# Performance work log

Measured on AMD Instinct MI355X. Metric: run time of the kernel, lower is better.

## Reference

```python
import jax, jax.numpy as jnp
import numpy as np

EMBED_DIM = 1024
NUM_HEADS = 16
HEAD_DIM = EMBED_DIM // NUM_HEADS  # 64
TOKEN_GRID = 48
TASK_ROPE_TOKENS = 8
SEQ_LEN = TASK_ROPE_TOKENS + TOKEN_GRID * TOKEN_GRID  # 2312
ROT_DIM = HEAD_DIM // 2  # 32, rotary 'dim' arg
SCALE = HEAD_DIM ** -0.5


def _make_rope_tables():
    # Faithful to RotaryEmbedding.__init__
    freqs = 1.0 / 10000.0 ** (jnp.arange(0, ROT_DIM, 2, dtype=jnp.float32) / float(ROT_DIM))
    t = jnp.arange(TOKEN_GRID, dtype=jnp.float32) / float(TOKEN_GRID) * float(TOKEN_GRID)
    freqs_1d = jnp.einsum('i,f->if', t, freqs)          # [G, ROT_DIM/2]
    freqs_1d = jnp.repeat(freqs_1d, 2, axis=-1)          # [G, ROT_DIM]
    fh = jnp.broadcast_to(freqs_1d[:, None, :], (TOKEN_GRID, TOKEN_GRID, ROT_DIM))
    fw = jnp.broadcast_to(freqs_1d[None, :, :], (TOKEN_GRID, TOKEN_GRID, ROT_DIM))
    freqs_2d = jnp.concatenate([fh, fw], axis=-1)        # [G, G, HEAD_DIM]
    freqs_flat = freqs_2d.reshape(TOKEN_GRID * TOKEN_GRID, -1)
    return jnp.cos(freqs_flat), jnp.sin(freqs_flat)      # each [G*G, HEAD_DIM]


def _rotate_half(x):
    x1, x2 = jnp.split(x, 2, axis=-1)
    return jnp.concatenate([-x2, x1], axis=-1)


def _apply_rope(t, cos, sin):
    # t: [H, L, D]; rotate tokens after the task prefix
    usable = t.shape[1] - TASK_ROPE_TOKENS
    c = cos[:usable, :HEAD_DIM]
    s = sin[:usable, :HEAD_DIM]
    to_rotate = t[:, TASK_ROPE_TOKENS:, :HEAD_DIM]
    rotated = to_rotate * c + _rotate_half(to_rotate) * s
    prefix = t[:, :TASK_ROPE_TOKENS, :HEAD_DIM]
    return jnp.concatenate([prefix, rotated], axis=1)


def setup_inputs() -> dict:
    key = jax.random.key(0)
    k1, k2, k3, k4, k5 = jax.random.split(key, 5)
    cos, sin = _make_rope_tables()
    bound = 1.0 / np.sqrt(EMBED_DIM)
    return {
        'x': jax.random.normal(k1, (SEQ_LEN, EMBED_DIM), dtype=jnp.float32),
        'key_padding_mask': jnp.ones((SEQ_LEN,), dtype=bool),
        'qkv_w': jax.random.uniform(k2, (3 * EMBED_DIM, EMBED_DIM), minval=-bound, maxval=bound, dtype=jnp.float32),
        'qkv_b': jax.random.uniform(k3, (3 * EMBED_DIM,), minval=-bound, maxval=bound, dtype=jnp.float32),
        'proj_w': jax.random.uniform(k4, (EMBED_DIM, EMBED_DIM), minval=-bound, maxval=bound, dtype=jnp.float32),
        'proj_b': jax.random.uniform(k5, (EMBED_DIM,), minval=-bound, maxval=bound, dtype=jnp.float32),
        'freqs_cos': cos,
        'freqs_sin': sin,
    }


def reference(x, key_padding_mask, qkv_w, qkv_b, proj_w, proj_b, freqs_cos, freqs_sin):
    L = x.shape[0]
    qkv = x @ qkv_w.T + qkv_b                             # [L, 3E]
    qkv = qkv.reshape(L, 3, NUM_HEADS, HEAD_DIM)
    qkv = jnp.transpose(qkv, (1, 2, 0, 3))                # [3, H, L, D]
    q, k, v = qkv[0], qkv[1], qkv[2]
    q = _apply_rope(q, freqs_cos, freqs_sin)
    k = _apply_rope(k, freqs_cos, freqs_sin)
    scores = jnp.einsum('hld,hmd->hlm', q, k) * SCALE     # [H, L, L]
    scores = jnp.where(key_padding_mask[None, None, :], scores, jnp.finfo(scores.dtype).min)
    weights = jax.nn.softmax(scores, axis=-1)
    context = jnp.einsum('hij,hjd->hid', weights, v)      # [H, L, D]
    context = jnp.transpose(context, (1, 0, 2)).reshape(L, -1)  # [L, E]
    out = context @ proj_w.T + proj_b
    return out
```

## Files before the change

### kernel.cpp

```cpp
#include <hip/hip_runtime.h>
#include <hip/hip_bf16.h>

#define SEQ   2312
#define EMB   1024
#define NH    16
#define HD    64
#define LP    2368
#define NKT   37
#define KSPLIT0 19
#define QKVN  3072
#define QSCALE 0.1803368801111713f

typedef __bf16 bf16x8 __attribute__((ext_vector_type(8)));
typedef __bf16 bf16x4 __attribute__((ext_vector_type(4)));
typedef _Float16 f16x8 __attribute__((ext_vector_type(8)));
typedef _Float16 f16x4 __attribute__((ext_vector_type(4)));
typedef float  f32x4  __attribute__((ext_vector_type(4)));

#define MFMA16(a,b,c) __builtin_amdgcn_mfma_f32_16x16x32_bf16((a),(b),(c),0,0,0)

#define N1 (SEQ * EMB / 4)
#define N2 (QKVN * EMB / 4)
#define N3 (EMB * EMB / 4)

__global__ __launch_bounds__(256) void cast_all_kernel(const float* __restrict__ x,
                                                       const float* __restrict__ qkv_w,
                                                       const float* __restrict__ proj_w,
                                                       __bf16* __restrict__ xb,
                                                       __bf16* __restrict__ wqkvb,
                                                       __bf16* __restrict__ wprojb) {
  int i = blockIdx.x * 256 + threadIdx.x;
  const float* src; __bf16* dst; int j;
  if (i < N1)           { src = x;      dst = xb;     j = i; }
  else if (i < N1 + N2) { src = qkv_w;  dst = wqkvb;  j = i - N1; }
  else if (i < N1 + N2 + N3) { src = proj_w; dst = wprojb; j = i - N1 - N2; }
  else return;
  const float4 v = reinterpret_cast<const float4*>(src)[j];
  bf16x4 o = { (__bf16)v.x, (__bf16)v.y, (__bf16)v.z, (__bf16)v.w };
  reinterpret_cast<bf16x4*>(dst)[j] = o;
}

__device__ __forceinline__ bf16x8 lds_frag(const __bf16* __restrict__ buf, int row, int cb) {
  const char* p = (const char*)buf + row * 128 + (cb ^ ((row & 7) << 4));
  return *reinterpret_cast<const bf16x8*>(p);
}

__device__ __forceinline__ void gl_lds16(const char* g, char* l) {
  __builtin_amdgcn_global_load_lds(
      (const __attribute__((address_space(1))) void*)g,
      (__attribute__((address_space(3))) void*)l, 16, 0, 0);
}

template <bool OUT_BF16>
__global__ __launch_bounds__(256) void gemm_lds_kernel(const __bf16* __restrict__ A,
                                                       const __bf16* __restrict__ B,
                                                       const float* __restrict__ bias,
                                                       void* __restrict__ Cout,
                                                       int M, int N, int K, int MT) {
  const int g = ((int)blockIdx.x & 7) * ((int)gridDim.x >> 3) + ((int)blockIdx.x >> 3);
  const int mt = g % MT, nt = g / MT;
  const int t = threadIdx.x;
  const int wid = t >> 6;
  const int lane = t & 63;
  const int lr = lane & 15, lg = lane >> 4;
  const int mrow = (wid >> 1) * 64, ncol = (wid & 1) * 64;

  __shared__ __bf16 sbuf[2][2][128 * 64];

  const int srow = t >> 3;
  const int ksw  = ((t & 7) ^ (srow & 7)) * 8;
  const __bf16* asrc[4]; const __bf16* bsrc[4];
#pragma unroll
  for (int i = 0; i < 4; ++i) {
    const int row = i * 32 + srow;
    int arow = mt * 128 + row; if (arow >= M) arow = M - 1;
    asrc[i] = A + (size_t)arow * K + ksw;
    bsrc[i] = B + (size_t)(nt * 128 + row) * K + ksw;
  }

  auto issue = [&](int buf, int kk) {
    char* ab = (char*)sbuf[buf][0] + wid * 1024;
    char* bb = (char*)sbuf[buf][1] + wid * 1024;
#pragma unroll
    for (int i = 0; i < 4; ++i) gl_lds16((const char*)(asrc[i] + kk), ab + i * 4096);
#pragma unroll
    for (int i = 0; i < 4; ++i) gl_lds16((const char*)(bsrc[i] + kk), bb + i * 4096);
  };

  f32x4 acc[4][4] = {};
  const int NK = K >> 6;
  issue(0, 0);

  for (int ks = 0; ks < NK; ++ks) {
    asm volatile("s_waitcnt vmcnt(0)" ::: "memory");
    __syncthreads();
    if (ks + 1 < NK) issue((ks + 1) & 1, (ks + 1) << 6);
    const __bf16* ab = sbuf[ks & 1][0];
    const __bf16* bb = sbuf[ks & 1][1];
#pragma unroll
    for (int kh2 = 0; kh2 < 2; ++kh2) {
      bf16x8 af[4], bf[4];
#pragma unroll
      for (int m = 0; m < 4; ++m) af[m] = lds_frag(ab, mrow + m * 16 + lr, kh2 * 64 + lg * 16);
#pragma unroll
      for (int n = 0; n < 4; ++n) bf[n] = lds_frag(bb, ncol + n * 16 + lr, kh2 * 64 + lg * 16);
#pragma unroll
      for (int m = 0; m < 4; ++m)
#pragma unroll
        for (int n = 0; n < 4; ++n)
          acc[m][n] = MFMA16(af[m], bf[n], acc[m][n]);
    }
    __syncthreads();
  }

#pragma unroll
  for (int m = 0; m < 4; ++m) {
#pragma unroll
    for (int n = 0; n < 4; ++n) {
#pragma unroll
      for (int r = 0; r < 4; ++r) {
        int row = mt * 128 + mrow + m * 16 + lg * 4 + r;
        int col = nt * 128 + ncol + n * 16 + lr;
        if (row < M) {
          float v = acc[m][n][r] + bias[col];
          if (OUT_BF16) reinterpret_cast<__bf16*>(Cout)[(size_t)row * N + col] = (__bf16)v;
          else          reinterpret_cast<float*>(Cout)[(size_t)row * N + col] = v;
        }
      }
    }
  }
}

__global__ __launch_bounds__(512) void gemm_qkv_kernel(const __bf16* __restrict__ A,
                                                       const __bf16* __restrict__ B,
                                                       const float* __restrict__ bias,
                                                       const float* __restrict__ fcos,
                                                       const float* __restrict__ fsin,
                                                       __bf16* __restrict__ qh,
                                                       __bf16* __restrict__ kh,
                                                       __bf16* __restrict__ vt) {
  const int g = ((int)blockIdx.x & 7) * 30 + ((int)blockIdx.x >> 3);
  const int mt = g % 10, nt = g / 10;
  const int t = threadIdx.x;
  const int wid = t >> 6;
  const int lane = t & 63;
  const int lr = lane & 15, lg = lane >> 4;
  const int mrow = (wid >> 1) * 64;
  const int ncol = (wid & 1) * 64;

  __shared__ __bf16 smem[49152];

  const int srow = t >> 3;
  const int ksw  = ((t & 7) ^ (srow & 7)) * 8;
  const __bf16* asrc[4]; const __bf16* bsrc[2];
#pragma unroll
  for (int i = 0; i < 4; ++i) {
    int arow = mt * 256 + i * 64 + srow; if (arow >= SEQ) arow = SEQ - 1;
    asrc[i] = A + (size_t)arow * EMB + ksw;
  }
#pragma unroll
  for (int i = 0; i < 2; ++i)
    bsrc[i] = B + (size_t)(nt * 128 + i * 64 + srow) * EMB + ksw;

  auto issue = [&](int buf, int kk) {
    char* ab = (char*)(smem + buf * 16384) + wid * 1024;
    char* bb = (char*)(smem + 32768 + buf * 8192) + wid * 1024;
#pragma unroll
    for (int i = 0; i < 4; ++i) gl_lds16((const char*)(asrc[i] + kk), ab + i * 8192);
#pragma unroll
    for (int i = 0; i < 2; ++i) gl_lds16((const char*)(bsrc[i] + kk), bb + i * 8192);
  };

  f32x4 acc[4][4] = {};
  issue(0, 0);

  for (int ks = 0; ks < 16; ++ks) {
    asm volatile("s_waitcnt vmcnt(0)" ::: "memory");
    __syncthreads();
    if (ks + 1 < 16) issue((ks + 1) & 1, (ks + 1) << 6);
    const __bf16* ab = smem + (ks & 1) * 16384;
    const __bf16* bb = smem + 32768 + (ks & 1) * 8192;
#pragma unroll
    for (int kh2 = 0; kh2 < 2; ++kh2) {
      bf16x8 af[4], bf[4];
#pragma unroll
      for (int m = 0; m < 4; ++m) af[m] = lds_frag(ab, mrow + m * 16 + lr, kh2 * 64 + lg * 16);
#pragma unroll
      for (int n = 0; n < 4; ++n) bf[n] = lds_frag(bb, ncol + n * 16 + lr, kh2 * 64 + lg * 16);
#pragma unroll
      for (int m = 0; m < 4; ++m)
#pragma unroll
        for (int n = 0; n < 4; ++n)
          acc[m][n] = MFMA16(af[m], bf[n], acc[m][n]);
    }
    __syncthreads();
  }

  const int colbase = nt * 128 + ncol;
  const int hb   = colbase >> 6;
  const int kind = hb >> 4;
  const int h    = hb & 15;
  float bb4[4];
#pragma unroll
  for (int n = 0; n < 4; ++n) bb4[n] = bias[colbase + n * 16 + lr];

  if (kind < 2) {
    __bf16* dst = (kind == 0 ? qh : kh) + (size_t)h * LP * 64;
    const float sc = (kind == 0) ? QSCALE : 1.0f;
#pragma unroll
    for (int m = 0; m < 4; ++m) {
#pragma unroll
      for (int r = 0; r < 4; ++r) {
        const int row = mt * 256 + mrow + m * 16 + lg * 4 + r;
        if (row >= SEQ) continue;
        float v0 = acc[m][0][r] + bb4[0];
        float v1 = acc[m][1][r] + bb4[1];
        float v2 = acc[m][2][r] + bb4[2];
        float v3 = acc[m][3][r] + bb4[3];
        if (row >= 8) {
          const float* cr = fcos + (size_t)(row - 8) * 64;
          const float* sr = fsin + (size_t)(row - 8) * 64;
          const float c0 = cr[lr],      s0 = sr[lr];
          const float c1 = cr[16 + lr], s1 = sr[16 + lr];
          const float c2 = cr[32 + lr], s2 = sr[32 + lr];
          const float c3 = cr[48 + lr], s3 = sr[48 + lr];
          const float o0 = v0 * c0 - v2 * s0;
          const float o2 = v2 * c2 + v0 * s2;
          const float o1 = v1 * c1 - v3 * s1;
          const float o3 = v3 * c3 + v1 * s3;
          v0 = o0; v1 = o1; v2 = o2; v3 = o3;
        }
        __bf16* p = dst + (size_t)row * 64;
        p[lr]      = (__bf16)(v0 * sc);
        p[16 + lr] = (__bf16)(v1 * sc);
        p[32 + lr] = (__bf16)(v2 * sc);
        p[48 + lr] = (__bf16)(v3 * sc);
      }
    }
  } else {
    __syncthreads();
    __bf16 (*vtile)[66] = reinterpret_cast<__bf16(*)[66]>(smem + wid * 64 * 66);
#pragma unroll
    for (int m = 0; m < 4; ++m)
#pragma unroll
      for (int r = 0; r < 4; ++r) {
        const int rl = m * 16 + lg * 4 + r;
#pragma unroll
        for (int n = 0; n < 4; ++n)
          vtile[rl][n * 16 + lr] = (__bf16)(acc[m][n][r] + bb4[n]);
      }
    __builtin_amdgcn_wave_barrier();
    const int pos = mt * 256 + mrow + lane;
    __bf16* vdst = vt + (size_t)h * 64 * LP;
    if (pos < LP) {
#pragma unroll 4
      for (int dl = 0; dl < 64; ++dl)
        vdst[(size_t)dl * LP + pos] = vtile[lane][dl];
    }
  }
}

__global__ __launch_bounds__(256) void flash_kernel(const __bf16* __restrict__ qh,
                                                    const __bf16* __restrict__ kh,
                                                    const __bf16* __restrict__ vt,
                                                    _Float16* __restrict__ Op,
                                                    float* __restrict__ lp) {
  const int g = (blockIdx.x & 7) * 148 + (blockIdx.x >> 3);
  const int h = g / 74;
  const int rem = g - h * 74;
  const int qb = rem >> 1, sp = rem & 1;
  const int kt0 = sp ? KSPLIT0 : 0, ktend = sp ? NKT : KSPLIT0;
  const int t = threadIdx.x;
  const int wid = t >> 6;
  const int lane = t & 63;
  const int lr = lane & 15, lg = lane >> 4;
  const int q0 = qb * 64 + wid * 16;

  __shared__ __bf16 kbuf[64 * 64];
  __shared__ __bf16 vbuf[64 * 64];
  __shared__ __bf16 plds[4][16][72];

  const __bf16* qbase = qh + ((size_t)h * LP + q0) * HD;
  const bf16x8 aq0 = *reinterpret_cast<const bf16x8*>(qbase + lr * HD + lg * 8);
  const bf16x8 aq1 = *reinterpret_cast<const bf16x8*>(qbase + lr * HD + 32 + lg * 8);

  const __bf16* khead = kh + (size_t)h * LP * HD;
  const __bf16* vhead = vt + (size_t)h * HD * LP;

  const int krow0 = t >> 3,        kcb0 = (t & 7) * 16;
  const int krow1 = 32 + (t >> 3);
  const int vrow  = t >> 2,        vcb0 = (t & 3) * 32;
  const int koff0 = krow0 * 128 + (kcb0 ^ ((krow0 & 7) << 4));
  const int koff1 = krow1 * 128 + (kcb0 ^ ((krow1 & 7) << 4));
  const int voff0 = vrow * 128 + (vcb0 ^ ((vrow & 7) << 4));
  const int voff1 = vrow * 128 + ((vcb0 + 16) ^ ((vrow & 7) << 4));
  const __bf16* vsrc = vhead + (size_t)vrow * LP + (t & 3) * 16;

  bf16x8 kreg0, kreg1, vreg0, vreg1;
  auto stage_load = [&](int kt) {
    const __bf16* kb = khead + (size_t)kt * 64 * HD;
    kreg0 = *reinterpret_cast<const bf16x8*>(kb + t * 8);
    kreg1 = *reinterpret_cast<const bf16x8*>(kb + 2048 + t * 8);
    vreg0 = *reinterpret_cast<const bf16x8*>(vsrc + kt * 64);
    vreg1 = *reinterpret_cast<const bf16x8*>(vsrc + kt * 64 + 8);
  };

  float l = 0.f;
  f32x4 oacc[4] = {};

  stage_load(kt0);

  for (int kt = kt0; kt < ktend; ++kt) {
    __syncthreads();
    *reinterpret_cast<bf16x8*>((char*)kbuf + koff0) = kreg0;
    *reinterpret_cast<bf16x8*>((char*)kbuf + koff1) = kreg1;
    *reinterpret_cast<bf16x8*>((char*)vbuf + voff0) = vreg0;
    *reinterpret_cast<bf16x8*>((char*)vbuf + voff1) = vreg1;
    __syncthreads();
    if (kt + 1 < ktend) stage_load(kt + 1);

    f32x4 sacc[4] = {};
    __builtin_amdgcn_s_setprio(1);
#pragma unroll
    for (int cg = 0; cg < 4; ++cg) {
      sacc[cg] = MFMA16(lds_frag(kbuf, cg * 16 + lr, lg * 16),      aq0, sacc[cg]);
      sacc[cg] = MFMA16(lds_frag(kbuf, cg * 16 + lr, 64 + lg * 16), aq1, sacc[cg]);
    }
    __builtin_amdgcn_s_setprio(0);
    if (kt == NKT - 1) {
#pragma unroll
      for (int cg = 0; cg < 4; ++cg)
#pragma unroll
        for (int r = 0; r < 4; ++r)
          if (kt * 64 + cg * 16 + lg * 4 + r >= SEQ) sacc[cg][r] = -1e30f;
    }
#pragma unroll
    for (int cg = 0; cg < 4; ++cg)
#pragma unroll
      for (int r = 0; r < 4; ++r) sacc[cg][r] = exp2f(sacc[cg][r]);
    float s0 = (sacc[0][0] + sacc[0][1]) + (sacc[0][2] + sacc[0][3]);
    float s1 = (sacc[1][0] + sacc[1][1]) + (sacc[1][2] + sacc[1][3]);
    float s2 = (sacc[2][0] + sacc[2][1]) + (sacc[2][2] + sacc[2][3]);
    float s3 = (sacc[3][0] + sacc[3][1]) + (sacc[3][2] + sacc[3][3]);
    l += (s0 + s1) + (s2 + s3);
#pragma unroll
    for (int cg = 0; cg < 4; ++cg) {
      bf16x4 pk = { (__bf16)sacc[cg][0], (__bf16)sacc[cg][1],
                    (__bf16)sacc[cg][2], (__bf16)sacc[cg][3] };
      *reinterpret_cast<bf16x4*>(&plds[wid][lr][cg * 16 + lg * 4]) = pk;
    }
    __builtin_amdgcn_wave_barrier();
    const bf16x8 ap0 = *reinterpret_cast<const bf16x8*>(&plds[wid][lr][lg * 8]);
    const bf16x8 ap1 = *reinterpret_cast<const bf16x8*>(&plds[wid][lr][32 + lg * 8]);
    __builtin_amdgcn_s_setprio(1);
#pragma unroll
    for (int cg = 0; cg < 4; ++cg) {
      oacc[cg] = MFMA16(lds_frag(vbuf, cg * 16 + lr, lg * 16),      ap0, oacc[cg]);
      oacc[cg] = MFMA16(lds_frag(vbuf, cg * 16 + lr, 64 + lg * 16), ap1, oacc[cg]);
    }
    __builtin_amdgcn_s_setprio(0);
  }
  float ltot = l;
  ltot += __shfl_xor(ltot, 16, 64);
  ltot += __shfl_xor(ltot, 32, 64);
  const float inv = 1.0f / ltot;
  const size_t rbase = ((size_t)sp * NH + h) * LP;
  if (lg == 0) lp[rbase + q0 + lr] = ltot;
  _Float16* orow = Op + (rbase + q0 + lr) * 64 + lg * 4;
#pragma unroll
  for (int cg = 0; cg < 4; ++cg) {
    f16x4 ov = { (_Float16)(oacc[cg][0] * inv), (_Float16)(oacc[cg][1] * inv),
                 (_Float16)(oacc[cg][2] * inv), (_Float16)(oacc[cg][3] * inv) };
    *reinterpret_cast<f16x4*>(orow + cg * 16) = ov;
  }
}

__global__ __launch_bounds__(256) void merge_kernel(const _Float16* __restrict__ Op,
                                                    const float* __restrict__ lp,
                                                    __bf16* __restrict__ ctx) {
  const int tg = blockIdx.x * 256 + threadIdx.x;
  const int rid = tg >> 2;
  const int d0 = (tg & 3) << 4;
  const int h = rid / LP;
  const int row = rid - h * LP;
  if (row >= SEQ) return;
  const size_t i0 = (size_t)h * LP + row;
  const size_t i1 = (size_t)NH * LP + i0;
  float w0 = lp[i0], w1 = lp[i1];
  const float inv = 1.0f / (w0 + w1);
  w0 *= inv; w1 *= inv;
  const f16x8* o0 = reinterpret_cast<const f16x8*>(Op + i0 * 64 + d0);
  const f16x8* o1 = reinterpret_cast<const f16x8*>(Op + i1 * 64 + d0);
  __bf16* co = ctx + (size_t)row * EMB + h * 64 + d0;
#pragma unroll
  for (int v = 0; v < 2; ++v) {
    const f16x8 a = o0[v], b = o1[v];
    bf16x8 o;
#pragma unroll
    for (int j = 0; j < 8; ++j)
      o[j] = (__bf16)((float)a[j] * w0 + (float)b[j] * w1);
    reinterpret_cast<bf16x8*>(co)[v] = o;
  }
}

extern "C" void kernel_launch(void* const* d_in, const int* in_sizes, int n_in,
                              void* d_out, int out_size, void* d_ws, size_t ws_size,
                              hipStream_t stream) {
  const float* x      = (const float*)d_in[0];
  const float* qkv_w  = (const float*)d_in[2];
  const float* qkv_b  = (const float*)d_in[3];
  const float* proj_w = (const float*)d_in[4];
  const float* proj_b = (const float*)d_in[5];
  const float* fcos   = (const float*)d_in[6];
  const float* fsin   = (const float*)d_in[7];
  float* out = (float*)d_out;

  char* ws = (char*)d_ws;
  size_t off = 0;
  auto alloc = [&](size_t bytes) {
    char* p = ws + off;
    off += (bytes + 255) & ~size_t(255);
    return p;
  };
  __bf16* xb     = (__bf16*)alloc((size_t)SEQ * EMB * 2);
  __bf16* wqkvb  = (__bf16*)alloc((size_t)QKVN * EMB * 2);
  __bf16* wprojb = (__bf16*)alloc((size_t)EMB * EMB * 2);
  __bf16* qh     = (__bf16*)alloc((size_t)NH * LP * HD * 2);
  __bf16* kh     = (__bf16*)alloc((size_t)NH * LP * HD * 2);
  __bf16* vtr    = (__bf16*)alloc((size_t)NH * HD * LP * 2);
  __bf16* ctx    = (__bf16*)alloc((size_t)SEQ * EMB * 2);
  _Float16* Op   = (_Float16*)alloc((size_t)2 * NH * LP * 64 * 2);
  float*    lpv  = (float*)alloc((size_t)2 * NH * LP * 4);

  cast_all_kernel<<<(N1 + N2 + N3 + 255) / 256, 256, 0, stream>>>(
      x, qkv_w, proj_w, xb, wqkvb, wprojb);

  gemm_qkv_kernel<<<240, 512, 0, stream>>>(xb, wqkvb, qkv_b, fcos, fsin, qh, kh, vtr);
  flash_kernel<<<1184, 256, 0, stream>>>(qh, kh, vtr, Op, lpv);
  merge_kernel<<<592, 256, 0, stream>>>(Op, lpv, ctx);
  gemm_lds_kernel<false><<<152, 256, 0, stream>>>(ctx, wprojb, proj_b, out,
                                                  SEQ, EMB, EMB, 19);
}
```

Before: 114.7 us.

## Fuse split-KV merge into output projection GEMM and compute row sums via MFMA

The separate merge kernel is removed, and the projection GEMM now loads both split-K partial outputs plus their softmax denominators, combines them in registers, and writes the merged bf16 A tile into LDS. This drops one launch and the ctx round trip through global memory. The A operand now goes through registers instead of direct global-to-LDS loads, which may add latency and register pressure. Separately, the flash kernel gets each softmax row sum from an extra pair of MFMAs against a ones vector, replacing the VALU adds and cross-lane shuffles.

```diff
diff --git a/kernel.cpp b/kernel.cpp
--- a/kernel.cpp
+++ b/kernel.cpp
@@ -49,86 +49,6 @@
   __builtin_amdgcn_global_load_lds(
       (const __attribute__((address_space(1))) void*)g,
       (__attribute__((address_space(3))) void*)l, 16, 0, 0);
-}
-
-template <bool OUT_BF16>
-__global__ __launch_bounds__(256) void gemm_lds_kernel(const __bf16* __restrict__ A,
-                                                       const __bf16* __restrict__ B,
-                                                       const float* __restrict__ bias,
-                                                       void* __restrict__ Cout,
-                                                       int M, int N, int K, int MT) {
-  const int g = ((int)blockIdx.x & 7) * ((int)gridDim.x >> 3) + ((int)blockIdx.x >> 3);
-  const int mt = g % MT, nt = g / MT;
-  const int t = threadIdx.x;
-  const int wid = t >> 6;
-  const int lane = t & 63;
-  const int lr = lane & 15, lg = lane >> 4;
-  const int mrow = (wid >> 1) * 64, ncol = (wid & 1) * 64;
-
-  __shared__ __bf16 sbuf[2][2][128 * 64];
-
-  const int srow = t >> 3;
-  const int ksw  = ((t & 7) ^ (srow & 7)) * 8;
-  const __bf16* asrc[4]; const __bf16* bsrc[4];
-#pragma unroll
-  for (int i = 0; i < 4; ++i) {
-    const int row = i * 32 + srow;
-    int arow = mt * 128 + row; if (arow >= M) arow = M - 1;
-    asrc[i] = A + (size_t)arow * K + ksw;
-    bsrc[i] = B + (size_t)(nt * 128 + row) * K + ksw;
-  }
-
-  auto issue = [&](int buf, int kk) {
-    char* ab = (char*)sbuf[buf][0] + wid * 1024;
-    char* bb = (char*)sbuf[buf][1] + wid * 1024;
-#pragma unroll
-    for (int i = 0; i < 4; ++i) gl_lds16((const char*)(asrc[i] + kk), ab + i * 4096);
-#pragma unroll
-    for (int i = 0; i < 4; ++i) gl_lds16((const char*)(bsrc[i] + kk), bb + i * 4096);
-  };
-
-  f32x4 acc[4][4] = {};
-  const int NK = K >> 6;
-  issue(0, 0);
-
-  for (int ks = 0; ks < NK; ++ks) {
-    asm volatile("s_waitcnt vmcnt(0)" ::: "memory");
-    __syncthreads();
-    if (ks + 1 < NK) issue((ks + 1) & 1, (ks + 1) << 6);
-    const __bf16* ab = sbuf[ks & 1][0];
-    const __bf16* bb = sbuf[ks & 1][1];
-#pragma unroll
-    for (int kh2 = 0; kh2 < 2; ++kh2) {
-      bf16x8 af[4], bf[4];
-#pragma unroll
-      for (int m = 0; m < 4; ++m) af[m] = lds_frag(ab, mrow + m * 16 + lr, kh2 * 64 + lg * 16);
-#pragma unroll
-      for (int n = 0; n < 4; ++n) bf[n] = lds_frag(bb, ncol + n * 16 + lr, kh2 * 64 + lg * 16);
-#pragma unroll
-      for (int m = 0; m < 4; ++m)
-#pragma unroll
-        for (int n = 0; n < 4; ++n)
-          acc[m][n] = MFMA16(af[m], bf[n], acc[m][n]);
-    }
-    __syncthreads();
-  }
-
-#pragma unroll
-  for (int m = 0; m < 4; ++m) {
-#pragma unroll
-    for (int n = 0; n < 4; ++n) {
-#pragma unroll
-      for (int r = 0; r < 4; ++r) {
-        int row = mt * 128 + mrow + m * 16 + lg * 4 + r;
-        int col = nt * 128 + ncol + n * 16 + lr;
-        if (row < M) {
-          float v = acc[m][n][r] + bias[col];
-          if (OUT_BF16) reinterpret_cast<__bf16*>(Cout)[(size_t)row * N + col] = (__bf16)v;
-          else          reinterpret_cast<float*>(Cout)[(size_t)row * N + col] = v;
-        }
-      }
-    }
-  }
 }
 
 __global__ __launch_bounds__(512) void gemm_qkv_kernel(const __bf16* __restrict__ A,
@@ -284,6 +204,9 @@
   const bf16x8 aq0 = *reinterpret_cast<const bf16x8*>(qbase + lr * HD + lg * 8);
   const bf16x8 aq1 = *reinterpret_cast<const bf16x8*>(qbase + lr * HD + 32 + lg * 8);
 
+  const bf16x8 vone = { (__bf16)1.f, (__bf16)1.f, (__bf16)1.f, (__bf16)1.f,
+                        (__bf16)1.f, (__bf16)1.f, (__bf16)1.f, (__bf16)1.f };
+
   const __bf16* khead = kh + (size_t)h * LP * HD;
   const __bf16* vhead = vt + (size_t)h * HD * LP;
 
@@ -305,7 +228,7 @@
     vreg1 = *reinterpret_cast<const bf16x8*>(vsrc + kt * 64 + 8);
   };
 
-  float l = 0.f;
+  f32x4 lacc = {};
   f32x4 oacc[4] = {};
 
   stage_load(kt0);
@@ -338,11 +261,6 @@
     for (int cg = 0; cg < 4; ++cg)
 #pragma unroll
       for (int r = 0; r < 4; ++r) sacc[cg][r] = exp2f(sacc[cg][r]);
-    float s0 = (sacc[0][0] + sacc[0][1]) + (sacc[0][2] + sacc[0][3]);
-    float s1 = (sacc[1][0] + sacc[1][1]) + (sacc[1][2] + sacc[1][3]);
-    float s2 = (sacc[2][0] + sacc[2][1]) + (sacc[2][2] + sacc[2][3]);
-    float s3 = (sacc[3][0] + sacc[3][1]) + (sacc[3][2] + sacc[3][3]);
-    l += (s0 + s1) + (s2 + s3);
 #pragma unroll
     for (int cg = 0; cg < 4; ++cg) {
       bf16x4 pk = { (__bf16)sacc[cg][0], (__bf16)sacc[cg][1],
@@ -358,11 +276,11 @@
       oacc[cg] = MFMA16(lds_frag(vbuf, cg * 16 + lr, lg * 16),      ap0, oacc[cg]);
       oacc[cg] = MFMA16(lds_frag(vbuf, cg * 16 + lr, 64 + lg * 16), ap1, oacc[cg]);
     }
+    lacc = MFMA16(vone, ap0, lacc);
+    lacc = MFMA16(vone, ap1, lacc);
     __builtin_amdgcn_s_setprio(0);
   }
-  float ltot = l;
-  ltot += __shfl_xor(ltot, 16, 64);
-  ltot += __shfl_xor(ltot, 32, 64);
+  const float ltot = lacc[0];
   const float inv = 1.0f / ltot;
   const size_t rbase = ((size_t)sp * NH + h) * LP;
   if (lg == 0) lp[rbase + q0 + lr] = ltot;
@@ -375,31 +293,105 @@
   }
 }
 
-__global__ __launch_bounds__(256) void merge_kernel(const _Float16* __restrict__ Op,
-                                                    const float* __restrict__ lp,
-                                                    __bf16* __restrict__ ctx) {
-  const int tg = blockIdx.x * 256 + threadIdx.x;
-  const int rid = tg >> 2;
-  const int d0 = (tg & 3) << 4;
-  const int h = rid / LP;
-  const int row = rid - h * LP;
-  if (row >= SEQ) return;
-  const size_t i0 = (size_t)h * LP + row;
-  const size_t i1 = (size_t)NH * LP + i0;
-  float w0 = lp[i0], w1 = lp[i1];
-  const float inv = 1.0f / (w0 + w1);
-  w0 *= inv; w1 *= inv;
-  const f16x8* o0 = reinterpret_cast<const f16x8*>(Op + i0 * 64 + d0);
-  const f16x8* o1 = reinterpret_cast<const f16x8*>(Op + i1 * 64 + d0);
-  __bf16* co = ctx + (size_t)row * EMB + h * 64 + d0;
-#pragma unroll
-  for (int v = 0; v < 2; ++v) {
-    const f16x8 a = o0[v], b = o1[v];
-    bf16x8 o;
-#pragma unroll
-    for (int j = 0; j < 8; ++j)
-      o[j] = (__bf16)((float)a[j] * w0 + (float)b[j] * w1);
-    reinterpret_cast<bf16x8*>(co)[v] = o;
+__global__ __launch_bounds__(256) void proj_merge_kernel(const _Float16* __restrict__ Op,
+                                                         const float* __restrict__ lp,
+                                                         const __bf16* __restrict__ B,
+                                                         const float* __restrict__ bias,
+                                                         float* __restrict__ Cout) {
+  const int g = ((int)blockIdx.x & 7) * 19 + ((int)blockIdx.x >> 3);
+  const int mt = g % 19, nt = g / 19;
+  const int t = threadIdx.x;
+  const int wid = t >> 6;
+  const int lane = t & 63;
+  const int lr = lane & 15, lg = lane >> 4;
+  const int mrow = (wid >> 1) * 64, ncol = (wid & 1) * 64;
+
+  __shared__ __bf16 sbuf[2][2][128 * 64];
+
+  const int srow = t >> 3;
+  const int ksw  = ((t & 7) ^ (srow & 7)) * 8;
+  int arows[4]; int adst[4]; const __bf16* bsrc[4];
+#pragma unroll
+  for (int i = 0; i < 4; ++i) {
+    const int row = i * 32 + srow;
+    int ar = mt * 128 + row; if (ar >= SEQ) ar = SEQ - 1;
+    arows[i] = ar;
+    adst[i] = row * 128 + (t & 7) * 16;
+    bsrc[i] = B + (size_t)(nt * 128 + row) * EMB + ksw;
+  }
+
+  auto issueB = [&](int buf, int kk) {
+    char* bb = (char*)sbuf[buf][1] + wid * 1024;
+#pragma unroll
+    for (int i = 0; i < 4; ++i) gl_lds16((const char*)(bsrc[i] + kk), bb + i * 4096);
+  };
+
+  f16x8 a0[4], a1[4]; float w0[4], w1[4];
+  auto loadA = [&](int ks) {
+#pragma unroll
+    for (int i = 0; i < 4; ++i) {
+      const size_t i0 = (size_t)ks * LP + arows[i];
+      const size_t i1 = (size_t)(NH + ks) * LP + arows[i];
+      a0[i] = *reinterpret_cast<const f16x8*>(Op + i0 * 64 + ksw);
+      a1[i] = *reinterpret_cast<const f16x8*>(Op + i1 * 64 + ksw);
+      w0[i] = lp[i0];
+      w1[i] = lp[i1];
+    }
+  };
+  auto writeA = [&](int buf) {
+#pragma unroll
+    for (int i = 0; i < 4; ++i) {
+      const float inv = 1.0f / (w0[i] + w1[i]);
+      const float u0 = w0[i] * inv, u1 = w1[i] * inv;
+      bf16x8 r;
+#pragma unroll
+      for (int j = 0; j < 8; ++j)
+        r[j] = (__bf16)((float)a0[i][j] * u0 + (float)a1[i][j] * u1);
+      *reinterpret_cast<bf16x8*>((char*)sbuf[buf][0] + adst[i]) = r;
+    }
+  };
+
+  f32x4 acc[4][4] = {};
+  loadA(0);
+  issueB(0, 0);
+  writeA(0);
+
+  for (int ks = 0; ks < 16; ++ks) {
+    asm volatile("s_waitcnt vmcnt(0)" ::: "memory");
+    __syncthreads();
+    const bool more = (ks + 1 < 16);
+    if (more) { issueB((ks + 1) & 1, (ks + 1) << 6); loadA(ks + 1); }
+    const __bf16* ab = sbuf[ks & 1][0];
+    const __bf16* bb = sbuf[ks & 1][1];
+#pragma unroll
+    for (int kh2 = 0; kh2 < 2; ++kh2) {
+      bf16x8 af[4], bf[4];
+#pragma unroll
+      for (int m = 0; m < 4; ++m) af[m] = lds_frag(ab, mrow + m * 16 + lr, kh2 * 64 + lg * 16);
+#pragma unroll
+      for (int n = 0; n < 4; ++n) bf[n] = lds_frag(bb, ncol + n * 16 + lr, kh2 * 64 + lg * 16);
+#pragma unroll
+      for (int m = 0; m < 4; ++m)
+#pragma unroll
+        for (int n = 0; n < 4; ++n)
+          acc[m][n] = MFMA16(af[m], bf[n], acc[m][n]);
+    }
+    if (more) writeA((ks + 1) & 1);
+    __syncthreads();
+  }
+
+#pragma unroll
+  for (int m = 0; m < 4; ++m) {
+#pragma unroll
+    for (int n = 0; n < 4; ++n) {
+#pragma unroll
+      for (int r = 0; r < 4; ++r) {
+        int row = mt * 128 + mrow + m * 16 + lg * 4 + r;
+        int col = nt * 128 + ncol + n * 16 + lr;
+        if (row < SEQ)
+          Cout[(size_t)row * EMB + col] = acc[m][n][r] + bias[col];
+      }
+    }
   }
 }
 
@@ -428,7 +420,6 @@
   __bf16* qh     = (__bf16*)alloc((size_t)NH * LP * HD * 2);
   __bf16* kh     = (__bf16*)alloc((size_t)NH * LP * HD * 2);
   __bf16* vtr    = (__bf16*)alloc((size_t)NH * HD * LP * 2);
-  __bf16* ctx    = (__bf16*)alloc((size_t)SEQ * EMB * 2);
   _Float16* Op   = (_Float16*)alloc((size_t)2 * NH * LP * 64 * 2);
   float*    lpv  = (float*)alloc((size_t)2 * NH * LP * 4);
 
@@ -437,7 +428,5 @@
 
   gemm_qkv_kernel<<<240, 512, 0, stream>>>(xb, wqkvb, qkv_b, fcos, fsin, qh, kh, vtr);
   flash_kernel<<<1184, 256, 0, stream>>>(qh, kh, vtr, Op, lpv);
-  merge_kernel<<<592, 256, 0, stream>>>(Op, lpv, ctx);
-  gemm_lds_kernel<false><<<152, 256, 0, stream>>>(ctx, wprojb, proj_b, out,
-                                                  SEQ, EMB, EMB, 19);
-}
+  proj_merge_kernel<<<152, 256, 0, stream>>>(Op, lpv, wprojb, proj_b, out);
+}
```

Measured after the change: 120.0 us. 4.7% more time.
